# Optimization experiments

Hardware: AMD Instinct MI355X
Metric: run time of the kernel (lower is better)

The kernel has to match this reference:

```python
import jax, jax.numpy as jnp
import numpy as np

V = 1024          # vocab_size
N = 500_000       # num automaton states
A = 16            # arcs per non-start state (start state has V dense arcs)
MAX_ORDER = 4     # max n-gram order -> max backoff chain length
START = 0         # start (unigram) state
B = 8192          # batch of hypotheses


def _build_automaton(seed=0):
    rng = np.random.default_rng(seed)
    num_arcs = V + (N - 1) * A
    arcs_weights = -(rng.random(num_arcs).astype(np.float32) * 8.0 + 0.05)
    to_states = rng.integers(0, N, num_arcs).astype(np.int32)
    ilabels = np.empty(num_arcs, np.int32)
    ilabels[:V] = np.arange(V, dtype=np.int32)  # start state: arc index == ilabel
    # unique sorted ilabels per non-start state
    base = rng.integers(0, V, N - 1).astype(np.int32)
    offs = np.arange(A, dtype=np.int32) * (V // A)
    ilabels[V:] = np.sort((base[:, None] + offs[None, :]) % V, axis=1).reshape(-1)
    state_start = np.empty(N, np.int32)
    state_end = np.empty(N, np.int32)
    state_start[0] = 0
    state_end[0] = V
    state_start[1:] = V + np.arange(N - 1, dtype=np.int32) * A
    state_end[1:] = state_start[1:] + A
    # state orders: start=1, rest in 2..MAX_ORDER; backoff goes to an order-(k-1) state
    order = np.empty(N, np.int64)
    order[0] = 1
    order[1:] = rng.integers(2, MAX_ORDER + 1, N - 1)
    order[1:MAX_ORDER] = np.arange(2, MAX_ORDER + 1)  # guarantee each order nonempty
    backoff_to = np.zeros(N, np.int32)               # order-2 states back off to START
    for k in range(3, MAX_ORDER + 1):
        mask = order == k
        prev = np.flatnonzero(order == k - 1)
        backoff_to[mask] = rng.choice(prev, mask.sum()).astype(np.int32)
    backoff_weights = -(rng.random(N).astype(np.float32) * 3.0)
    backoff_weights[0] = 0.0
    return dict(
        arcs_weights=jnp.asarray(arcs_weights),
        backoff_weights=jnp.asarray(backoff_weights),
        ilabels=jnp.asarray(ilabels),
        to_states=jnp.asarray(to_states),
        backoff_to_states=jnp.asarray(backoff_to),
        state_start_arcs=jnp.asarray(state_start),
        state_end_arcs=jnp.asarray(state_end),
    )


def setup_inputs() -> dict:
    key = jax.random.key(0)
    inp = _build_automaton(0)
    inp["states"] = jax.random.randint(key, (B,), 0, N, dtype=jnp.int32)
    return inp


def _advance(states, arcs_weights, backoff_weights, ilabels, to_states,
             backoff_to_states, state_start_arcs, state_end_arcs):
    b = states.shape[0]
    rows = jnp.arange(b)[:, None]
    # column V is a dump slot for masked-out scatters
    scores_e = jnp.zeros((b, V + 1), arcs_weights.dtype)
    next_e = jnp.zeros((b, V + 1), jnp.int32)
    found_e = jnp.zeros((b, V + 1), bool)
    cur = states.astype(jnp.int32)
    acc = jnp.zeros((b,), arcs_weights.dtype)  # accumulated backoff weight
    offs = jnp.arange(A, dtype=jnp.int32)
    for _ in range(MAX_ORDER - 1):  # chase backoffs down to the start state
        at_start = cur == START
        idx = state_start_arcs[cur][:, None] + offs                    # [b, A]
        valid = (idx < state_end_arcs[cur][:, None]) & (~at_start)[:, None]
        idx = jnp.where(valid, idx, 0)
        lab = ilabels[idx]                                             # [b, A]
        can = valid & ~jnp.take_along_axis(found_e, lab, axis=1)
        slot = jnp.where(can, lab, V)
        scores_e = scores_e.at[rows, slot].set(acc[:, None] + arcs_weights[idx])
        next_e = next_e.at[rows, slot].set(to_states[idx])
        found_e = found_e.at[rows, slot].set(True)
        acc = jnp.where(at_start, acc, acc + backoff_weights[cur])
        cur = jnp.where(at_start, cur, backoff_to_states[cur])
    # start state has a dense arc table: arc index == ilabel for 0..V-1
    nf = ~found_e[:, :V]
    scores = jnp.where(nf, acc[:, None] + arcs_weights[None, :V], scores_e[:, :V])
    next_states = jnp.where(nf, to_states[None, :V], next_e[:, :V])
    return scores, next_states


def reference(states, arcs_weights, backoff_weights, ilabels, to_states,
              backoff_to_states, state_start_arcs, state_end_arcs):
    return _advance(states, arcs_weights, backoff_weights, ilabels, to_states,
                    backoff_to_states, state_start_arcs, state_end_arcs)
```

## Files before the change

kernel.cpp:

```cpp
#include <hip/hip_runtime.h>

#define VOCAB 1024
#define ARCS  16
#define CHAIN 3
#define START_STATE 0
#define WAVE 64
#define WAVES_PER_BLOCK 4
#define BLOCK (WAVE * WAVES_PER_BLOCK)
#define NCHUNK (VOCAB / (WAVE * 4))

typedef float f32x4 __attribute__((ext_vector_type(4)));
typedef int   i32x4 __attribute__((ext_vector_type(4)));

__global__ __launch_bounds__(BLOCK, 8) void ngram_advance_kernel(
    const float* __restrict__ arcs_weights,
    const float* __restrict__ backoff_weights,
    const int*   __restrict__ ilabels,
    const int*   __restrict__ to_states,
    const int*   __restrict__ backoff_to,
    const int*   __restrict__ state_start,
    const int*   __restrict__ state_end,
    const int*   __restrict__ states,
    float*       __restrict__ out_scores,
    float*       __restrict__ out_next,
    int B)
{
    __shared__ unsigned char s_who[WAVES_PER_BLOCK][VOCAB];

    const int lane = threadIdx.x & (WAVE - 1);
    const int wid  = __builtin_amdgcn_readfirstlane(threadIdx.x >> 6);
    const int b    = blockIdx.x * WAVES_PER_BLOCK + wid;
    if (b >= B) return;

    unsigned char* __restrict__ who = s_who[wid];

    int cur = states[b];

    *(i32x4*)&who[lane * 16] = (i32x4){-1, -1, -1, -1};

    float acc = 0.0f;
    const int   cs0 = cur;  const float ca0 = acc;
    acc += backoff_weights[cur];  cur = backoff_to[cur];
    const int   cs1 = cur;  const float ca1 = acc;
    acc += backoff_weights[cur];  cur = backoff_to[cur];
    const int   cs2 = cur;  const float ca2 = acc;
    acc += backoff_weights[cur];
    const float accf = acc;

    const int level = lane >> 4;
    const int arc   = lane & (ARCS - 1);
    int   lab = -1;
    float sc  = 0.0f, fns = 0.0f;
    bool  ok  = false;
    if (lane < CHAIN * ARCS) {
        const int   s    = (level == 0) ? cs0 : (level == 1) ? cs1 : cs2;
        const float cacc = (level == 0) ? ca0 : (level == 1) ? ca1 : ca2;
        if (s != START_STATE) {
            const int idx = state_start[s] + arc;
            if (idx < state_end[s]) {
                lab = ilabels[idx];
                sc  = cacc + arcs_weights[idx];
                fns = (float)to_states[idx];
                ok  = true;
            }
        }
    }

    if (ok && level == 2) who[lab] = (unsigned char)lane;
    __builtin_amdgcn_sched_barrier(0);
    if (ok && level == 1) who[lab] = (unsigned char)lane;
    __builtin_amdgcn_sched_barrier(0);
    if (ok && level == 0) who[lab] = (unsigned char)lane;
    __builtin_amdgcn_sched_barrier(0);

    float* __restrict__ so = out_scores + (size_t)b * VOCAB;
    float* __restrict__ no = out_next   + (size_t)b * VOCAB;
    const int sci = __float_as_int(sc);
    const int nsi = __float_as_int(fns);
    #pragma unroll
    for (int i = 0; i < NCHUNK; ++i) {
        const int v = (lane + i * WAVE) * 4;
        const unsigned w4 = *(const unsigned*)&who[v];
        const f32x4 dwv = *(const f32x4*)&arcs_weights[v];
        const i32x4 dnv = *(const i32x4*)&to_states[v];
        f32x4 rs, rx;
        #pragma unroll
        for (int j = 0; j < 4; ++j) {
            const unsigned wb = (w4 >> (8 * j)) & 0xFFu;
            const float scv = __int_as_float(
                __builtin_amdgcn_ds_bpermute((int)(wb << 2), sci));
            const float nsv = __int_as_float(
                __builtin_amdgcn_ds_bpermute((int)(wb << 2), nsi));
            const bool hit = (wb != 0xFFu);
            rs[j] = hit ? scv : accf + dwv[j];
            rx[j] = hit ? nsv : (float)dnv[j];
        }
        *(f32x4*)&so[v] = rs;
        *(f32x4*)&no[v] = rx;
    }
}

extern "C" void kernel_launch(void* const* d_in, const int* in_sizes, int n_in,
                              void* d_out, int out_size, void* d_ws, size_t ws_size,
                              hipStream_t stream) {
    const float* arcs_weights    = (const float*)d_in[0];
    const float* backoff_weights = (const float*)d_in[1];
    const int*   ilabels         = (const int*)d_in[2];
    const int*   to_states       = (const int*)d_in[3];
    const int*   backoff_to      = (const int*)d_in[4];
    const int*   state_start     = (const int*)d_in[5];
    const int*   state_end       = (const int*)d_in[6];
    const int*   states          = (const int*)d_in[7];

    const int B = in_sizes[7];
    float* out_scores = (float*)d_out;
    float* out_next   = out_scores + (size_t)B * VOCAB;

    const int grid = (B + WAVES_PER_BLOCK - 1) / WAVES_PER_BLOCK;
    ngram_advance_kernel<<<grid, BLOCK, 0, stream>>>(
        arcs_weights, backoff_weights, ilabels, to_states, backoff_to,
        state_start, state_end, states, out_scores, out_next, B);
}
```

Before: 19.38 us.

## Split each hypothesis row across four waves, one vocab quarter each

```diff
diff --git a/kernel.cpp b/kernel.cpp
--- a/kernel.cpp
+++ b/kernel.cpp
@@ -7,7 +7,7 @@
 #define WAVE 64
 #define WAVES_PER_BLOCK 4
 #define BLOCK (WAVE * WAVES_PER_BLOCK)
-#define NCHUNK (VOCAB / (WAVE * 4))
+#define QUART (VOCAB / WAVES_PER_BLOCK)
 
 typedef float f32x4 __attribute__((ext_vector_type(4)));
 typedef int   i32x4 __attribute__((ext_vector_type(4)));
@@ -22,21 +22,21 @@
     const int*   __restrict__ state_end,
     const int*   __restrict__ states,
     float*       __restrict__ out_scores,
-    float*       __restrict__ out_next,
-    int B)
+    float*       __restrict__ out_next)
 {
-    __shared__ unsigned char s_who[WAVES_PER_BLOCK][VOCAB];
+    __shared__ unsigned char s_who[WAVES_PER_BLOCK][QUART];
 
     const int lane = threadIdx.x & (WAVE - 1);
     const int wid  = __builtin_amdgcn_readfirstlane(threadIdx.x >> 6);
-    const int b    = blockIdx.x * WAVES_PER_BLOCK + wid;
-    if (b >= B) return;
+    const int b    = blockIdx.x;
+    const int base = wid * QUART;
 
     unsigned char* __restrict__ who = s_who[wid];
 
     int cur = states[b];
 
-    *(i32x4*)&who[lane * 16] = (i32x4){-1, -1, -1, -1};
+    *(unsigned*)&who[lane * 4] = 0xFFFFFFFFu;
+    __builtin_amdgcn_sched_barrier(0);
 
     float acc = 0.0f;
     const int   cs0 = cur;  const float ca0 = acc;
@@ -65,39 +65,35 @@
             }
         }
     }
+    const unsigned lv = (unsigned)(lab - base);
 
-    if (ok && level == 2) who[lab] = (unsigned char)lane;
+    if (ok && level == 2 && lv < QUART) who[lv] = (unsigned char)lane;
     __builtin_amdgcn_sched_barrier(0);
-    if (ok && level == 1) who[lab] = (unsigned char)lane;
+    if (ok && level == 1 && lv < QUART) who[lv] = (unsigned char)lane;
     __builtin_amdgcn_sched_barrier(0);
-    if (ok && level == 0) who[lab] = (unsigned char)lane;
+    if (ok && level == 0 && lv < QUART) who[lv] = (unsigned char)lane;
     __builtin_amdgcn_sched_barrier(0);
 
-    float* __restrict__ so = out_scores + (size_t)b * VOCAB;
-    float* __restrict__ no = out_next   + (size_t)b * VOCAB;
+    const int gv = base + lane * 4;
+    const unsigned w4 = *(const unsigned*)&who[lane * 4];
+    const f32x4 dwv = *(const f32x4*)&arcs_weights[gv];
+    const i32x4 dnv = *(const i32x4*)&to_states[gv];
     const int sci = __float_as_int(sc);
     const int nsi = __float_as_int(fns);
+    f32x4 rs, rx;
     #pragma unroll
-    for (int i = 0; i < NCHUNK; ++i) {
-        const int v = (lane + i * WAVE) * 4;
-        const unsigned w4 = *(const unsigned*)&who[v];
-        const f32x4 dwv = *(const f32x4*)&arcs_weights[v];
-        const i32x4 dnv = *(const i32x4*)&to_states[v];
-        f32x4 rs, rx;
-        #pragma unroll
-        for (int j = 0; j < 4; ++j) {
-            const unsigned wb = (w4 >> (8 * j)) & 0xFFu;
-            const float scv = __int_as_float(
-                __builtin_amdgcn_ds_bpermute((int)(wb << 2), sci));
-            const float nsv = __int_as_float(
-                __builtin_amdgcn_ds_bpermute((int)(wb << 2), nsi));
-            const bool hit = (wb != 0xFFu);
-            rs[j] = hit ? scv : accf + dwv[j];
-            rx[j] = hit ? nsv : (float)dnv[j];
-        }
-        *(f32x4*)&so[v] = rs;
-        *(f32x4*)&no[v] = rx;
+    for (int j = 0; j < 4; ++j) {
+        const unsigned wb = (w4 >> (8 * j)) & 0xFFu;
+        const float scv = __int_as_float(
+            __builtin_amdgcn_ds_bpermute((int)(wb << 2), sci));
+        const float nsv = __int_as_float(
+            __builtin_amdgcn_ds_bpermute((int)(wb << 2), nsi));
+        const bool hit = (wb != 0xFFu);
+        rs[j] = hit ? scv : accf + dwv[j];
+        rx[j] = hit ? nsv : (float)dnv[j];
     }
+    *(f32x4*)&out_scores[(size_t)b * VOCAB + gv] = rs;
+    *(f32x4*)&out_next  [(size_t)b * VOCAB + gv] = rx;
 }
 
 extern "C" void kernel_launch(void* const* d_in, const int* in_sizes, int n_in,
@@ -116,8 +112,7 @@
     float* out_scores = (float*)d_out;
     float* out_next   = out_scores + (size_t)B * VOCAB;
 
-    const int grid = (B + WAVES_PER_BLOCK - 1) / WAVES_PER_BLOCK;
-    ngram_advance_kernel<<<grid, BLOCK, 0, stream>>>(
+    ngram_advance_kernel<<<B, BLOCK, 0, stream>>>(
         arcs_weights, backoff_weights, ilabels, to_states, backoff_to,
-        state_start, state_end, states, out_scores, out_next, B);
+        state_start, state_end, states, out_scores, out_next);
 }
```

Result: slower. 20.87 us (+7.7%).

## Split advance into overlay-build and streaming-merge kernels via workspace

Applied to the files above, without the earlier changes.

```diff
diff --git a/kernel.cpp b/kernel.cpp
--- a/kernel.cpp
+++ b/kernel.cpp
@@ -8,11 +8,137 @@
 #define WAVES_PER_BLOCK 4
 #define BLOCK (WAVE * WAVES_PER_BLOCK)
 #define NCHUNK (VOCAB / (WAVE * 4))
+#define SLOTS (CHAIN * ARCS)
 
 typedef float f32x4 __attribute__((ext_vector_type(4)));
 typedef int   i32x4 __attribute__((ext_vector_type(4)));
 
-__global__ __launch_bounds__(BLOCK, 8) void ngram_advance_kernel(
+__global__ __launch_bounds__(BLOCK, 8) void build_overlay_kernel(
+    const float* __restrict__ arcs_weights,
+    const float* __restrict__ backoff_weights,
+    const int*   __restrict__ ilabels,
+    const int*   __restrict__ to_states,
+    const int*   __restrict__ backoff_to,
+    const int*   __restrict__ state_start,
+    const int*   __restrict__ state_end,
+    const int*   __restrict__ states,
+    int*         __restrict__ ws_lab,
+    float*       __restrict__ ws_sc,
+    float*       __restrict__ ws_ns,
+    float*       __restrict__ ws_accf,
+    int B)
+{
+    const int lane = threadIdx.x & (WAVE - 1);
+    const int wid  = __builtin_amdgcn_readfirstlane(threadIdx.x >> 6);
+    const int b    = blockIdx.x * WAVES_PER_BLOCK + wid;
+    if (b >= B) return;
+
+    int cur = states[b];
+    float acc = 0.0f;
+    const int   cs0 = cur;  const float ca0 = acc;
+    acc += backoff_weights[cur];  cur = backoff_to[cur];
+    const int   cs1 = cur;  const float ca1 = acc;
+    acc += backoff_weights[cur];  cur = backoff_to[cur];
+    const int   cs2 = cur;  const float ca2 = acc;
+    acc += backoff_weights[cur];
+    const float accf = acc;
+
+    const int level = lane >> 4;
+    const int arc   = lane & (ARCS - 1);
+    int   lab = -1;
+    float sc  = 0.0f, fns = 0.0f;
+    bool  ok  = false;
+    if (lane < SLOTS) {
+        const int   s    = (level == 0) ? cs0 : (level == 1) ? cs1 : cs2;
+        const float cacc = (level == 0) ? ca0 : (level == 1) ? ca1 : ca2;
+        if (s != START_STATE) {
+            const int idx = state_start[s] + arc;
+            if (idx < state_end[s]) {
+                lab = ilabels[idx];
+                sc  = cacc + arcs_weights[idx];
+                fns = (float)to_states[idx];
+                ok  = true;
+            }
+        }
+    }
+
+    int kill = 0;
+    #pragma unroll
+    for (int k = 0; k < 2 * ARCS; ++k) {
+        const int lk = __builtin_amdgcn_readlane(lab, k);
+        if (k < ARCS) kill |= (int)(level >= 1) & (int)(lab == lk);
+        else          kill |= (int)(level == 2) & (int)(lab == lk);
+    }
+
+    if (lane < SLOTS) {
+        const int slot = b * SLOTS + lane;
+        ws_lab[slot] = (ok && !kill) ? lab : -1;
+        ws_sc [slot] = sc;
+        ws_ns [slot] = fns;
+    }
+    if (lane == 0) ws_accf[b] = accf;
+}
+
+__global__ __launch_bounds__(BLOCK, 8) void stream_merge_kernel(
+    const float* __restrict__ arcs_weights,
+    const int*   __restrict__ to_states,
+    const int*   __restrict__ ws_lab,
+    const float* __restrict__ ws_sc,
+    const float* __restrict__ ws_ns,
+    const float* __restrict__ ws_accf,
+    float*       __restrict__ out_scores,
+    float*       __restrict__ out_next,
+    int B)
+{
+    __shared__ unsigned char s_who[WAVES_PER_BLOCK][VOCAB];
+
+    const int lane = threadIdx.x & (WAVE - 1);
+    const int wid  = __builtin_amdgcn_readfirstlane(threadIdx.x >> 6);
+    const int b    = blockIdx.x * WAVES_PER_BLOCK + wid;
+    if (b >= B) return;
+
+    unsigned char* __restrict__ who = s_who[wid];
+
+    int lab = -1, sci = 0, nsi = 0;
+    if (lane < SLOTS) {
+        const int slot = b * SLOTS + lane;
+        lab = ws_lab[slot];
+        sci = __float_as_int(ws_sc[slot]);
+        nsi = __float_as_int(ws_ns[slot]);
+    }
+    const float accf = ws_accf[b];
+
+    *(i32x4*)&who[lane * 16] = (i32x4){-1, -1, -1, -1};
+    __builtin_amdgcn_sched_barrier(0);
+    if (lab >= 0) who[lab] = (unsigned char)lane;
+    __builtin_amdgcn_sched_barrier(0);
+
+    float* __restrict__ so = out_scores + (size_t)b * VOCAB;
+    float* __restrict__ no = out_next   + (size_t)b * VOCAB;
+    #pragma unroll
+    for (int i = 0; i < NCHUNK; ++i) {
+        const int v = (lane + i * WAVE) * 4;
+        const unsigned w4 = *(const unsigned*)&who[v];
+        const f32x4 dwv = *(const f32x4*)&arcs_weights[v];
+        const i32x4 dnv = *(const i32x4*)&to_states[v];
+        f32x4 rs, rx;
+        #pragma unroll
+        for (int j = 0; j < 4; ++j) {
+            const unsigned wb = (w4 >> (8 * j)) & 0xFFu;
+            const float scv = __int_as_float(
+                __builtin_amdgcn_ds_bpermute((int)(wb << 2), sci));
+            const float nsv = __int_as_float(
+                __builtin_amdgcn_ds_bpermute((int)(wb << 2), nsi));
+            const bool hit = (wb != 0xFFu);
+            rs[j] = hit ? scv : accf + dwv[j];
+            rx[j] = hit ? nsv : (float)dnv[j];
+        }
+        *(f32x4*)&so[v] = rs;
+        *(f32x4*)&no[v] = rx;
+    }
+}
+
+__global__ __launch_bounds__(BLOCK, 8) void ngram_fused_kernel(
     const float* __restrict__ arcs_weights,
     const float* __restrict__ backoff_weights,
     const int*   __restrict__ ilabels,
@@ -33,9 +159,7 @@
     if (b >= B) return;
 
     unsigned char* __restrict__ who = s_who[wid];
-
     int cur = states[b];
-
     *(i32x4*)&who[lane * 16] = (i32x4){-1, -1, -1, -1};
 
     float acc = 0.0f;
@@ -52,7 +176,7 @@
     int   lab = -1;
     float sc  = 0.0f, fns = 0.0f;
     bool  ok  = false;
-    if (lane < CHAIN * ARCS) {
+    if (lane < SLOTS) {
         const int   s    = (level == 0) ? cs0 : (level == 1) ? cs1 : cs2;
         const float cacc = (level == 0) ? ca0 : (level == 1) ? ca1 : ca2;
         if (s != START_STATE) {
@@ -116,8 +240,27 @@
     float* out_scores = (float*)d_out;
     float* out_next   = out_scores + (size_t)B * VOCAB;
 
-    const int grid = (B + WAVES_PER_BLOCK - 1) / WAVES_PER_BLOCK;
-    ngram_advance_kernel<<<grid, BLOCK, 0, stream>>>(
-        arcs_weights, backoff_weights, ilabels, to_states, backoff_to,
-        state_start, state_end, states, out_scores, out_next, B);
-}
+    const int    grid   = (B + WAVES_PER_BLOCK - 1) / WAVES_PER_BLOCK;
+    const size_t needed = (size_t)B * SLOTS * 4 * 3 + (size_t)B * 4;
+
+    if (ws_size >= needed) {
+        char* ws = (char*)d_ws;
+        int*   ws_lab  = (int*)ws;
+        float* ws_sc   = (float*)(ws + (size_t)B * SLOTS * 4);
+        float* ws_ns   = (float*)(ws + (size_t)B * SLOTS * 8);
+        float* ws_accf = (float*)(ws + (size_t)B * SLOTS * 12);
+
+        build_overlay_kernel<<<grid, BLOCK, 0, stream>>>(
+            arcs_weights, backoff_weights, ilabels, to_states, backoff_to,
+            state_start, state_end, states,
+            ws_lab, ws_sc, ws_ns, ws_accf, B);
+        stream_merge_kernel<<<grid, BLOCK, 0, stream>>>(
+            arcs_weights, to_states,
+            ws_lab, ws_sc, ws_ns, ws_accf,
+            out_scores, out_next, B);
+    } else {
+        ngram_fused_kernel<<<grid, BLOCK, 0, stream>>>(
+            arcs_weights, backoff_weights, ilabels, to_states, backoff_to,
+            state_start, state_end, states, out_scores, out_next, B);
+    }
+}
```

Measured after the change: 23.92 us. 1.23x slower.
